# Optimization experiments

Measured on AMD Instinct MI355X. Metric: run time of the kernel, lower is better.

The kernel has to match this reference:

```python
import jax, jax.numpy as jnp
import numpy as np

U, I, E, D, R = 100000, 50000, 2000000, 64, 5


def setup_inputs() -> dict:
    key = jax.random.key(0)
    ks = jax.random.split(key, 14)
    def n(k, shape, scale=0.05):
        return jax.random.normal(k, shape, jnp.float32) * scale
    return {
        "user_feat": n(ks[0], (U, D), 1.0),
        "item_feat": n(ks[1], (I, D), 1.0),
        "rating_feat": n(ks[2], (R, D), 1.0),
        "row_idxs": jax.random.randint(ks[3], (E,), 0, I),   # item index per edge
        "col_idxs": jax.random.randint(ks[4], (E,), 0, U),   # user index per edge (dst)
        "rating": jax.random.randint(ks[5], (E,), 0, R),
        # gv = Linear(2D,D)+ReLU -> Linear(D,D)+ReLU
        "gv_w1": n(ks[6], (2 * D, D)), "gv_b1": jnp.zeros((D,), jnp.float32),
        "gv_w2": n(ks[7], (D, D)),     "gv_b2": jnp.zeros((D,), jnp.float32),
        # Attention: Linear(2D,D)+ReLU -> Linear(D,D)+ReLU -> Linear(D,1)
        "att_w1": n(ks[8], (2 * D, D)), "att_b1": jnp.zeros((D,), jnp.float32),
        "att_w2": n(ks[9], (D, D)),     "att_b2": jnp.zeros((D,), jnp.float32),
        "att_w3": n(ks[10], (D, 1)),    "att_b3": jnp.zeros((1,), jnp.float32),
        # output projection w = Linear(D,D)
        "w_w": n(ks[11], (D, D)), "w_b": jnp.zeros((D,), jnp.float32),
    }


def segment_softmax(logits, seg, num_segments):
    # numerically stable softmax over edges grouped by destination node
    m = jax.ops.segment_max(logits, seg, num_segments=num_segments)
    e = jnp.exp(logits - m[seg])
    s = jax.ops.segment_sum(e, seg, num_segments=num_segments)
    return e / s[seg]


def reference(user_feat, item_feat, rating_feat, row_idxs, col_idxs, rating,
              gv_w1, gv_b1, gv_w2, gv_b2,
              att_w1, att_b1, att_w2, att_b2, att_w3, att_b3,
              w_w, w_b):
    # gather per-edge embeddings
    r_emb = rating_feat[rating]          # [E, D]
    i_emb = item_feat[row_idxs]          # [E, D]
    u_emb = user_feat[col_idxs]          # [E, D]
    # gv MLP on concat(item, rating)
    x = jnp.concatenate([i_emb, r_emb], axis=1)              # [E, 2D]
    h1 = jax.nn.relu(x @ gv_w1 + gv_b1)
    x_ia = jax.nn.relu(h1 @ gv_w2 + gv_b2)                   # [E, D]
    # attention MLP on concat(x_ia, user)
    a = jnp.concatenate([x_ia, u_emb], axis=1)               # [E, 2D]
    a = jax.nn.relu(a @ att_w1 + att_b1)
    a = jax.nn.relu(a @ att_w2 + att_b2)
    weight = (a @ att_w3 + att_b3)[:, 0]                     # [E]
    # edge_softmax over incoming edges of each destination (user) node
    value = segment_softmax(weight, col_idxs, U)             # [E]
    # scatter-sum weighted messages to users
    h = jax.ops.segment_sum(x_ia * value[:, None], col_idxs, num_segments=U)  # [U, D]
    # act is None -> plain linear
    return h @ w_w + w_b
```

## Files before the change

### kernel.cpp

```cpp
#include <hip/hip_runtime.h>
#include <hip/hip_bf16.h>
#include <hip/hip_fp8.h>

#define U_N 100000
#define I_N 50000
#define E_N 2000000
#define R_N 5
#define C_N (I_N*R_N)
#define NBLK_U 391
#define NBLK_E 7813
#define NBLK_C 1954
#define NBUCKC 196

typedef __hip_bfloat16 bf16_t;
typedef unsigned short u16;
typedef unsigned char u8;
typedef __attribute__((ext_vector_type(8))) short bf16x8;
typedef __attribute__((ext_vector_type(4))) float f32x4;

__device__ __forceinline__ float blo(unsigned u){ return __uint_as_float(u<<16); }
__device__ __forceinline__ float bhi(unsigned u){ return __uint_as_float(u & 0xffff0000u); }
__device__ __forceinline__ unsigned pkbf(float a, float b){
  __hip_bfloat162 t = __float22bfloat162_rn(float2{a,b});
  union { __hip_bfloat162 h; unsigned u; } cv; cv.h = t; return cv.u;
}
__device__ __forceinline__ u16 f2b(float v){
  union { __hip_bfloat16 h; u16 u; } cv; cv.h = __float2bfloat16(v); return cv.u;
}
__device__ __forceinline__ float f8f(unsigned b){
  __hip_fp8_e4m3 h; h.__x = (u8)b; return (float)h;
}
__device__ __forceinline__ unsigned ff8(float f){
  __hip_fp8_e4m3 h(f); return (unsigned)h.__x;
}

__global__ __launch_bounds__(256) void k_histQ(const int* __restrict__ cols, int* __restrict__ hist_g){
  __shared__ int histI[NBUCKC];
  int t = threadIdx.x, b = blockIdx.x;
  if(t < NBUCKC) histI[t] = 0;
  __syncthreads();
  int e = b*256 + t;
  if(e < E_N) atomicAdd(&histI[cols[e] >> 9], 1);
  __syncthreads();
  if(t < NBUCKC) hist_g[(size_t)b*NBUCKC + t] = histI[t];
}

__global__ __launch_bounds__(256) void k_scanQ(const int* __restrict__ hist_g, int* __restrict__ boff_g,
                                               int* __restrict__ qtot){
  __shared__ int wsum[4];
  int t = threadIdx.x, q = blockIdx.x;
  int lane = t & 63, wv = t >> 6;
  int running = 0;
  for(int c0=0; c0<NBLK_E; c0+=256){
    int b = c0 + t;
    int v = (b < NBLK_E) ? hist_g[(size_t)b*NBUCKC + q] : 0;
    int inc = v;
#pragma unroll
    for(int off=1; off<64; off<<=1){
      int x = __shfl(inc, lane-off);
      if(lane >= off) inc += x;
    }
    if(lane == 63) wsum[wv] = inc;
    __syncthreads();
    int w0=wsum[0], w1=wsum[1], w2=wsum[2], w3=wsum[3];
    int wpre = (wv>0?w0:0) + (wv>1?w1:0) + (wv>2?w2:0);
    if(b < NBLK_E) boff_g[(size_t)b*NBUCKC + q] = running + wpre + inc - v;
    running += w0 + w1 + w2 + w3;
    __syncthreads();
  }
  if(t == 0) qtot[q] = running;
}

__global__ void k_scanT(const int* __restrict__ qtot, int* __restrict__ qbase){
  __shared__ int s[256];
  int t = threadIdx.x;
  int v = (t < NBUCKC) ? qtot[t] : 0;
  s[t] = v; __syncthreads();
  for(int off=1; off<256; off<<=1){
    int x = (t>=off) ? s[t-off] : 0;
    __syncthreads();
    s[t] += x;
    __syncthreads();
  }
  if(t < NBUCKC) qbase[t] = s[t] - v;
  if(t == 255)   qbase[NBUCKC] = s[255];
}

__global__ __launch_bounds__(256) void k_blockq(const int* __restrict__ qbase, int* __restrict__ blockq){
  int b = blockIdx.x*256 + threadIdx.x; if(b >= NBLK_E) return;
  int e = b*256;
  int lo = 0, hi = NBUCKC-1;
  while(lo < hi){ int mid = (lo+hi+1)>>1; if(qbase[mid] <= e) lo = mid; else hi = mid-1; }
  blockq[b] = lo;
}

__global__ __launch_bounds__(256) void k_place2(const int* __restrict__ rows, const int* __restrict__ cols,
                                                const int* __restrict__ rats,
                                                const int* __restrict__ boff_g, const int* __restrict__ qbase,
                                                unsigned* __restrict__ uc2){
  __shared__ int rankI[NBUCKC];
  __shared__ int baseI[NBUCKC];
  int t = threadIdx.x, b = blockIdx.x;
  if(t < NBUCKC){
    rankI[t] = 0;
    baseI[t] = qbase[t] + boff_g[(size_t)b*NBUCKC + t];
  }
  __syncthreads();
  int e = b*256 + t;
  if(e < E_N){
    int u = cols[e];
    int c = rows[e]*5 + rats[e];
    int q = u >> 9;
    int r = atomicAdd(&rankI[q], 1);
    uc2[baseI[q] + r] = ((unsigned)(u & 16383) << 18) | (unsigned)c;
  }
}

__global__ __launch_bounds__(256) void k_fineB1(const unsigned* __restrict__ uc2, const int* __restrict__ qbase,
                                                int* __restrict__ cnt){
  __shared__ int hist[512];
  int t = threadIdx.x, q = blockIdx.x;
  hist[t] = 0; hist[t+256] = 0;
  __syncthreads();
  int r0 = qbase[q], r1 = qbase[q+1];
  for(int j=r0+t; j<r1; j+=256) atomicAdd(&hist[(uc2[j]>>18) & 511], 1);
  __syncthreads();
  cnt[q*512 + t]       = hist[t];
  cnt[q*512 + t + 256] = hist[t+256];
}

__global__ __launch_bounds__(256) void k_scanA(const int* __restrict__ cnt, int* __restrict__ start,
                                               int* __restrict__ bsum){
  __shared__ int s[256];
  int t = threadIdx.x, i = blockIdx.x*256 + t;
  int v = (i < U_N) ? cnt[i] : 0;
  s[t] = v; __syncthreads();
  for(int off=1; off<256; off<<=1){
    int x = (t>=off) ? s[t-off] : 0;
    __syncthreads();
    s[t] += x;
    __syncthreads();
  }
  start[i] = s[t] - v;
  if(t == 255) bsum[blockIdx.x] = s[255];
}

__global__ void k_scanB(int* bsum, int n){
  __shared__ int s[512];
  int t = threadIdx.x;
  int v = (t < n) ? bsum[t] : 0;
  s[t] = v; __syncthreads();
  for(int off=1; off<512; off<<=1){
    int x = (t>=off) ? s[t-off] : 0;
    __syncthreads();
    s[t] += x;
    __syncthreads();
  }
  if(t < n) bsum[t] = s[t] - v;
}

__global__ __launch_bounds__(256) void k_scanC(int* start, const int* __restrict__ bsum){
  int i = blockIdx.x*256 + threadIdx.x;
  start[i] += bsum[blockIdx.x];
}

__global__ __launch_bounds__(256) void k_fineB2(const unsigned* __restrict__ uc2, const int* __restrict__ qbase,
                                                const int* __restrict__ start,
                                                unsigned* __restrict__ uc3){
  __shared__ int fillb[512];
  __shared__ int startb[512];
  int t = threadIdx.x, q = blockIdx.x;
  fillb[t] = 0; fillb[t+256] = 0;
  startb[t]     = start[q*512 + t];
  startb[t+256] = start[q*512 + t + 256];
  __syncthreads();
  int r0 = qbase[q], r1 = qbase[q+1];
  for(int j=r0+t; j<r1; j+=256){
    unsigned v = uc2[j];
    int ul = (int)((v>>18) & 511);
    int off = atomicAdd(&fillb[ul], 1);
    uc3[startb[ul] + off] = v;
  }
}

__global__ void k_ratpart(const float* __restrict__ rf, const float* __restrict__ w1,
                          const float* __restrict__ b1, float* __restrict__ out){
  int t = threadIdx.x; if(t >= R_N*64) return;
  int r = t>>6, d = t&63;
  float acc = b1[d];
  for(int k=0;k<64;k++) acc += rf[r*64 + k] * w1[(64+k)*64 + d];
  out[t] = acc;
}

__global__ __launch_bounds__(256) void k_prepw6(const float* __restrict__ w1, const float* __restrict__ a1,
                                                const float* __restrict__ w2, const float* __restrict__ a2,
                                                const float* __restrict__ ww,
                                                u16* w1t, u16* u1t, u16* w2t, u16* a1t, u16* a2t, u16* wwt){
  int idx = (blockIdx.x & 15)*256 + threadIdx.x;
  int sec = blockIdx.x >> 4;
  int d = idx >> 6, k = idx & 63;
  const float* src; u16* dst; int ko = 0;
  switch(sec){
    case 0: src=w1; dst=w1t; break;
    case 1: src=a1; dst=u1t; ko=64; break;
    case 2: src=w2; dst=w2t; break;
    case 3: src=a1; dst=a1t; break;
    case 4: src=a2; dst=a2t; break;
    default: src=ww; dst=wwt; break;
  }
  dst[idx] = f2b(src[(size_t)(ko+k)*64 + d]);
}

template<bool BIAS>
__global__ __launch_bounds__(256) void k_rowgemm(const float4* __restrict__ in,
                                                 const uint4* __restrict__ wt,
                                                 const float* __restrict__ bias,
                                                 uint4* __restrict__ outp, int n){
  __shared__ uint4 A_u4[2048];
  __shared__ uint4 W_u4[512];
  __shared__ float bsh[64];
  u16* A16 = (u16*)A_u4;
  const int tid = threadIdx.x;
  for(int cid = tid; cid < 512; cid += 256){
    int dd = cid >> 3, ch = cid & 7;
    W_u4[dd*8 + (ch ^ (dd&7))] = wt[cid];
  }
  if(BIAS && tid < 64) bsh[tid] = bias[tid];
  const int base = blockIdx.x*256;
  const int ch = tid & 7;
#pragma unroll
  for(int it=0; it<8; ++it){
    int s = it*32 + (tid>>3);
    int r = base + s;
    uint4 o = {0,0,0,0};
    if(r < n){
      const float4* p = in + (size_t)r*16 + ch*2;
      float4 v0 = p[0], v1 = p[1];
      o.x = pkbf(v0.x, v0.y); o.y = pkbf(v0.z, v0.w);
      o.z = pkbf(v1.x, v1.y); o.w = pkbf(v1.z, v1.w);
    }
    A_u4[s*8 + (ch ^ (s&7))] = o;
  }
  __syncthreads();
  const int l = tid & 63, w = tid >> 6;
  const int lr = l & 15, g = l >> 4;
  bf16x8 bfr[4][2];
#pragma unroll
  for(int nt=0; nt<4; ++nt)
#pragma unroll
    for(int kk=0; kk<2; ++kk){
      int d = nt*16 + lr;
      bfr[nt][kk] = *(const bf16x8*)&W_u4[d*8 + ((kk*4+g) ^ (d&7))];
    }
  float bv[4];
#pragma unroll
  for(int nt=0; nt<4; ++nt) bv[nt] = BIAS ? bsh[nt*16 + lr] : 0.f;
#pragma unroll
  for(int t=0; t<4; ++t){
    int s = w*64 + t*16 + lr;
    bf16x8 af0 = *(const bf16x8*)&A_u4[s*8 + ((0*4+g) ^ (s&7))];
    bf16x8 af1 = *(const bf16x8*)&A_u4[s*8 + ((1*4+g) ^ (s&7))];
    f32x4 acc[4];
#pragma unroll
    for(int nt=0; nt<4; ++nt){
      f32x4 c0 = { bv[nt], bv[nt], bv[nt], bv[nt] };
      c0 = __builtin_amdgcn_mfma_f32_16x16x32_bf16(af0, bfr[nt][0], c0, 0, 0, 0);
      c0 = __builtin_amdgcn_mfma_f32_16x16x32_bf16(af1, bfr[nt][1], c0, 0, 0, 0);
      acc[nt] = c0;
    }
#pragma unroll
    for(int nt=0; nt<4; ++nt){
      int d = nt*16 + lr;
#pragma unroll
      for(int reg=0; reg<4; ++reg){
        int srow = w*64 + t*16 + g*4 + reg;
        A16[srow*64 + ((d>>3)^(srow&7))*8 + (d&7)] = f2b(acc[nt][reg]);
      }
    }
  }
#pragma unroll
  for(int it=0; it<8; ++it){
    int s = w*64 + it*8 + (l>>3);
    int c2 = l & 7;
    int r = base + s;
    if(r < n) outp[(size_t)r*8 + c2] = A_u4[s*8 + (c2 ^ (s&7))];
  }
}

__global__ __launch_bounds__(256) void k_combo_mfma(const uint4* __restrict__ itemp,
                                                    const float4* __restrict__ ratp,
                                                    const uint4* __restrict__ w2t_g, const uint4* __restrict__ a1t_g,
                                                    const uint4* __restrict__ wwt_g,
                                                    const float* __restrict__ b2,
                                                    uint4* __restrict__ y_o, u8* __restrict__ xa1_o8){
  __shared__ uint4 A_u4[1024];
  __shared__ uint4 X_u4[1024];
  __shared__ uint4 W2_u4[512];
  __shared__ uint4 A1_u4[512];
  __shared__ uint4 WW_u4[512];
  __shared__ float4 rsh4[80];
  __shared__ float b2sh[64];
  u16* A16 = (u16*)A_u4;
  u16* X16 = (u16*)X_u4;
  const int tid = threadIdx.x;
  for(int cid = tid; cid < 512; cid += 256){
    int dd = cid >> 3, ch = cid & 7;
    W2_u4[dd*8 + (ch ^ (dd&7))] = w2t_g[cid];
    A1_u4[dd*8 + (ch ^ (dd&7))] = a1t_g[cid];
    WW_u4[dd*8 + (ch ^ (dd&7))] = wwt_g[cid];
  }
  if(tid < 80) rsh4[tid] = ratp[tid];
  if(tid < 64) b2sh[tid] = b2[tid];
  __syncthreads();

  const int base = blockIdx.x*128;
  const int ch = tid & 7;
#pragma unroll
  for(int it=0; it<4; ++it){
    int s = it*32 + (tid>>3);
    int cidx = base + s;
    uint4 o = {0,0,0,0};
    if(cidx < C_N){
      int i = cidx/5, r = cidx - i*5;
      uint4 iv = itemp[(size_t)i*8 + ch];
      float4 r0 = rsh4[r*16 + ch*2], r1 = rsh4[r*16 + ch*2 + 1];
      o.x = pkbf(fmaxf(blo(iv.x)+r0.x,0.f), fmaxf(bhi(iv.x)+r0.y,0.f));
      o.y = pkbf(fmaxf(blo(iv.y)+r0.z,0.f), fmaxf(bhi(iv.y)+r0.w,0.f));
      o.z = pkbf(fmaxf(blo(iv.z)+r1.x,0.f), fmaxf(bhi(iv.z)+r1.y,0.f));
      o.w = pkbf(fmaxf(blo(iv.w)+r1.z,0.f), fmaxf(bhi(iv.w)+r1.w,0.f));
    }
    A_u4[s*8 + (ch ^ (s&7))] = o;
  }
  __syncthreads();

  const int l = tid & 63, w = tid >> 6;
  const int lr = l & 15, g = l >> 4;
  bf16x8 w2f[4][2], a1f[4][2], wwf[4][2];
#pragma unroll
  for(int nt=0; nt<4; ++nt)
#pragma unroll
    for(int kk=0; kk<2; ++kk){
      int d = nt*16 + lr;
      w2f[nt][kk] = *(const bf16x8*)&W2_u4[d*8 + ((kk*4+g) ^ (d&7))];
      a1f[nt][kk] = *(const bf16x8*)&A1_u4[d*8 + ((kk*4+g) ^ (d&7))];
      wwf[nt][kk] = *(const bf16x8*)&WW_u4[d*8 + ((kk*4+g) ^ (d&7))];
    }
  float b2v[4];
#pragma unroll
  for(int nt=0; nt<4; ++nt) b2v[nt] = b2sh[nt*16 + lr];

#pragma unroll
  for(int t=0; t<2; ++t){
    int s = w*32 + t*16 + lr;
    bf16x8 af0 = *(const bf16x8*)&A_u4[s*8 + ((0*4+g) ^ (s&7))];
    bf16x8 af1 = *(const bf16x8*)&A_u4[s*8 + ((1*4+g) ^ (s&7))];
#pragma unroll
    for(int nt=0; nt<4; ++nt){
      f32x4 c0 = { b2v[nt], b2v[nt], b2v[nt], b2v[nt] };
      c0 = __builtin_amdgcn_mfma_f32_16x16x32_bf16(af0, w2f[nt][0], c0, 0, 0, 0);
      c0 = __builtin_amdgcn_mfma_f32_16x16x32_bf16(af1, w2f[nt][1], c0, 0, 0, 0);
      int d = nt*16 + lr;
#pragma unroll
      for(int reg=0; reg<4; ++reg){
        int srow = w*32 + t*16 + g*4 + reg;
        X16[srow*64 + ((d>>3)^(srow&7))*8 + (d&7)] = f2b(fmaxf(c0[reg], 0.f));
      }
    }
    bf16x8 xf0 = *(const bf16x8*)&X_u4[s*8 + ((0*4+g) ^ (s&7))];
    bf16x8 xf1 = *(const bf16x8*)&X_u4[s*8 + ((1*4+g) ^ (s&7))];
#pragma unroll
    for(int nt=0; nt<4; ++nt){
      f32x4 c0 = { 0.f, 0.f, 0.f, 0.f };
      c0 = __builtin_amdgcn_mfma_f32_16x16x32_bf16(xf0, a1f[nt][0], c0, 0, 0, 0);
      c0 = __builtin_amdgcn_mfma_f32_16x16x32_bf16(xf1, a1f[nt][1], c0, 0, 0, 0);
      int d = nt*16 + lr;
#pragma unroll
      for(int reg=0; reg<4; ++reg){
        int srow = w*32 + t*16 + g*4 + reg;
        A16[srow*64 + ((d>>3)^(srow&7))*8 + (d&7)] = f2b(c0[reg]);
      }
    }
#pragma unroll
    for(int nt=0; nt<4; ++nt){
      f32x4 c0 = { 0.f, 0.f, 0.f, 0.f };
      c0 = __builtin_amdgcn_mfma_f32_16x16x32_bf16(xf0, wwf[nt][0], c0, 0, 0, 0);
      c0 = __builtin_amdgcn_mfma_f32_16x16x32_bf16(xf1, wwf[nt][1], c0, 0, 0, 0);
      int d = nt*16 + lr;
#pragma unroll
      for(int reg=0; reg<4; ++reg){
        int srow = w*32 + t*16 + g*4 + reg;
        X16[srow*64 + ((d>>3)^(srow&7))*8 + (d&7)] = f2b(c0[reg]);
      }
    }
  }
#pragma unroll
  for(int it=0; it<4; ++it){
    int s = w*32 + it*8 + (l>>3);
    int c2 = l & 7;
    int r = base + s;
    if(r < C_N) y_o[(size_t)r*8 + c2] = X_u4[s*8 + (c2 ^ (s&7))];
  }
#pragma unroll
  for(int it=0; it<2; ++it){
    int slot = it*64 + l;
    int rl = slot >> 2;
    int c4 = slot & 3;
    int s = w*32 + rl;
    int r = base + s;
    if(r < C_N){
      uint4 h0 = A_u4[s*8 + ((c4*2+0) ^ (s&7))];
      uint4 h1 = A_u4[s*8 + ((c4*2+1) ^ (s&7))];
      uint4 o;
      o.x = ff8(blo(h0.x)) | (ff8(bhi(h0.x))<<8) | (ff8(blo(h0.y))<<16) | (ff8(bhi(h0.y))<<24);
      o.y = ff8(blo(h0.z)) | (ff8(bhi(h0.z))<<8) | (ff8(blo(h0.w))<<16) | (ff8(bhi(h0.w))<<24);
      o.z = ff8(blo(h1.x)) | (ff8(bhi(h1.x))<<8) | (ff8(blo(h1.y))<<16) | (ff8(bhi(h1.y))<<24);
      o.w = ff8(blo(h1.z)) | (ff8(bhi(h1.z))<<8) | (ff8(blo(h1.w))<<16) | (ff8(bhi(h1.w))<<24);
      *(uint4*)(xa1_o8 + (size_t)r*64 + c4*16) = o;
    }
  }
}

__global__ __launch_bounds__(256) void k_edge_mfma(const unsigned* __restrict__ uc3,
                                                   const int* __restrict__ qbase, const int* __restrict__ blockq,
                                                   const u8* __restrict__ xa1p8, const uint4* __restrict__ userp,
                                                   const u16* __restrict__ w2t_g,
                                                   const float* __restrict__ a2b,
                                                   const float* __restrict__ a3w, const float* __restrict__ a3b,
                                                   float* __restrict__ wlog){
  const int tid = threadIdx.x;
  const int base = blockIdx.x*256;
  const int l = tid & 63, w = tid >> 6;
  const int lr = l & 15;
  const int g  = l >> 4;
  bf16x8 bf[4][2];
#pragma unroll
  for(int nt=0; nt<4; ++nt)
#pragma unroll
    for(int kk=0; kk<2; ++kk){
      int d = nt*16 + lr;
      bf[nt][kk] = *(const bf16x8*)(w2t_g + d*64 + kk*32 + g*8);
    }
  float b2v[4], a3v[4];
#pragma unroll
  for(int nt=0; nt<4; ++nt){ b2v[nt] = a2b[nt*16 + lr]; a3v[nt] = a3w[nt*16 + lr]; }
  const float a3b0 = a3b[0];

  int cin[4], uin[4];
  int bq = blockq[blockIdx.x];
#pragma unroll
  for(int t=0; t<4; ++t){
    int s = base + w*64 + t*16 + lr;
    int sc = (s < E_N) ? s : (E_N-1);
    unsigned vv = (s < E_N) ? uc3[s] : 0u;
    int q = bq;
    while(sc >= qbase[q+1]) ++q;
    cin[t] = (int)(vv & 0x3FFFFu);
    uin[t] = (q<<9) | (int)((vv>>18) & 511u);
  }

  auto compute = [&](uint2 xq0, uint2 xq1, uint4 uv0, uint4 uv1, int t){
    union { uint4 u4; bf16x8 v; } a0, a1;
    a0.u4.x = pkbf(fmaxf(f8f(xq0.x&255u)+blo(uv0.x),0.f),       fmaxf(f8f((xq0.x>>8)&255u)+bhi(uv0.x),0.f));
    a0.u4.y = pkbf(fmaxf(f8f((xq0.x>>16)&255u)+blo(uv0.y),0.f), fmaxf(f8f(xq0.x>>24)+bhi(uv0.y),0.f));
    a0.u4.z = pkbf(fmaxf(f8f(xq0.y&255u)+blo(uv0.z),0.f),       fmaxf(f8f((xq0.y>>8)&255u)+bhi(uv0.z),0.f));
    a0.u4.w = pkbf(fmaxf(f8f((xq0.y>>16)&255u)+blo(uv0.w),0.f), fmaxf(f8f(xq0.y>>24)+bhi(uv0.w),0.f));
    a1.u4.x = pkbf(fmaxf(f8f(xq1.x&255u)+blo(uv1.x),0.f),       fmaxf(f8f((xq1.x>>8)&255u)+bhi(uv1.x),0.f));
    a1.u4.y = pkbf(fmaxf(f8f((xq1.x>>16)&255u)+blo(uv1.y),0.f), fmaxf(f8f(xq1.x>>24)+bhi(uv1.y),0.f));
    a1.u4.z = pkbf(fmaxf(f8f(xq1.y&255u)+blo(uv1.z),0.f),       fmaxf(f8f((xq1.y>>8)&255u)+bhi(uv1.z),0.f));
    a1.u4.w = pkbf(fmaxf(f8f((xq1.y>>16)&255u)+blo(uv1.w),0.f), fmaxf(f8f(xq1.y>>24)+bhi(uv1.w),0.f));
    f32x4 acc[4];
#pragma unroll
    for(int nt=0; nt<4; ++nt){
      f32x4 c0 = { b2v[nt], b2v[nt], b2v[nt], b2v[nt] };
      c0 = __builtin_amdgcn_mfma_f32_16x16x32_bf16(a0.v, bf[nt][0], c0, 0, 0, 0);
      c0 = __builtin_amdgcn_mfma_f32_16x16x32_bf16(a1.v, bf[nt][1], c0, 0, 0, 0);
      acc[nt] = c0;
    }
    float s0=0.f, s1=0.f, s2=0.f, s3=0.f;
#pragma unroll
    for(int nt=0; nt<4; ++nt){
      s0 += fmaxf(acc[nt][0], 0.f) * a3v[nt];
      s1 += fmaxf(acc[nt][1], 0.f) * a3v[nt];
      s2 += fmaxf(acc[nt][2], 0.f) * a3v[nt];
      s3 += fmaxf(acc[nt][3], 0.f) * a3v[nt];
    }
#pragma unroll
    for(int mask=1; mask<16; mask<<=1){
      s0 += __shfl_xor(s0, mask);
      s1 += __shfl_xor(s1, mask);
      s2 += __shfl_xor(s2, mask);
      s3 += __shfl_xor(s3, mask);
    }
    if(lr == 0){
      int e0 = base + w*64 + t*16 + g*4;
      if(e0+0 < E_N) wlog[e0+0] = s0 + a3b0;
      if(e0+1 < E_N) wlog[e0+1] = s1 + a3b0;
      if(e0+2 < E_N) wlog[e0+2] = s2 + a3b0;
      if(e0+3 < E_N) wlog[e0+3] = s3 + a3b0;
    }
  };

  uint2 xA0 = *(const uint2*)(xa1p8 + (size_t)cin[0]*64 + g*8);
  uint2 xA1 = *(const uint2*)(xa1p8 + (size_t)cin[0]*64 + 32 + g*8);
  uint4 uA0 = userp[(size_t)uin[0]*8 + g];
  uint4 uA1 = userp[(size_t)uin[0]*8 + 4 + g];
  uint2 xB0 = *(const uint2*)(xa1p8 + (size_t)cin[1]*64 + g*8);
  uint2 xB1 = *(const uint2*)(xa1p8 + (size_t)cin[1]*64 + 32 + g*8);
  uint4 uB0 = userp[(size_t)uin[1]*8 + g];
  uint4 uB1 = userp[(size_t)uin[1]*8 + 4 + g];

  compute(xA0, xA1, uA0, uA1, 0);
  xA0 = *(const uint2*)(xa1p8 + (size_t)cin[2]*64 + g*8);
  xA1 = *(const uint2*)(xa1p8 + (size_t)cin[2]*64 + 32 + g*8);
  uA0 = userp[(size_t)uin[2]*8 + g];
  uA1 = userp[(size_t)uin[2]*8 + 4 + g];
  compute(xB0, xB1, uB0, uB1, 1);
  xB0 = *(const uint2*)(xa1p8 + (size_t)cin[3]*64 + g*8);
  xB1 = *(const uint2*)(xa1p8 + (size_t)cin[3]*64 + 32 + g*8);
  uB0 = userp[(size_t)uin[3]*8 + g];
  uB1 = userp[(size_t)uin[3]*8 + 4 + g];
  compute(xA0, xA1, uA0, uA1, 2);
  compute(xB0, xB1, uB0, uB1, 3);
}

__global__ __launch_bounds__(256) void k_aggf(const int* __restrict__ start,
                                              const unsigned* __restrict__ uc3,
                                              const float* __restrict__ wlog,
                                              const u16* __restrict__ Y,
                                              const float* __restrict__ wb,
                                              float* __restrict__ out){
  __shared__ uint4 Ysh[2][4][256];
  int w = threadIdx.x >> 6, l = threadIdx.x & 63;
  int lr = l & 15, g = l >> 4;
  int base = (blockIdx.x*4 + w) * 16;
  if(base >= U_N) return;
  int s0g = start[base];
  int s1g = start[base+16];
  unsigned ml = (unsigned)((base + lr) & 16383);
  int sA = s0g & ~31;
  int nch = (s1g - sA + 31) >> 5;
  const int kb = g*8;

  float m = -1e30f;
  for(int ch=0; ch<nch; ++ch){
    int e0 = sA + ch*32;
    float4 wv0 = *(const float4*)(wlog + e0 + kb);
    float4 wv1 = *(const float4*)(wlog + e0 + kb + 4);
    uint4 v0 = *(const uint4*)(uc3 + e0 + kb);
    uint4 v1 = *(const uint4*)(uc3 + e0 + kb + 4);
    if((v0.x>>18)==ml) m = fmaxf(m, wv0.x);
    if((v0.y>>18)==ml) m = fmaxf(m, wv0.y);
    if((v0.z>>18)==ml) m = fmaxf(m, wv0.z);
    if((v0.w>>18)==ml) m = fmaxf(m, wv0.w);
    if((v1.x>>18)==ml) m = fmaxf(m, wv1.x);
    if((v1.y>>18)==ml) m = fmaxf(m, wv1.y);
    if((v1.z>>18)==ml) m = fmaxf(m, wv1.z);
    if((v1.w>>18)==ml) m = fmaxf(m, wv1.w);
  }
  m = fmaxf(m, __shfl_xor(m, 16));
  m = fmaxf(m, __shfl_xor(m, 32));

  f32x4 acc[4];
#pragma unroll
  for(int nt=0; nt<4; ++nt) acc[nt] = f32x4{0.f,0.f,0.f,0.f};
  float ssum = 0.f;
  int buf = 0;
  if(nch > 0){
    int rowe = sA + (l>>1);
    int crow = (int)(uc3[rowe] & 0x3FFFFu);
    const uint4* yp = (const uint4*)Y + (size_t)crow*8 + (l&1)*4;
    uint4 y0=yp[0], y1=yp[1], y2=yp[2], y3=yp[3];
    uint4* dst = &Ysh[0][w][(l>>1)*8 + (l&1)*4];
    dst[0]=y0; dst[1]=y1; dst[2]=y2; dst[3]=y3;
  }
  for(int ch=0; ch<nch; ++ch){
    int e0 = sA + ch*32;
    uint4 n0, n1, n2, n3;
    bool hasNext = (ch+1 < nch);
    if(hasNext){
      int rowe = e0 + 32 + (l>>1);
      int crowN = (int)(uc3[rowe] & 0x3FFFFu);
      const uint4* yp = (const uint4*)Y + (size_t)crowN*8 + (l&1)*4;
      n0=yp[0]; n1=yp[1]; n2=yp[2]; n3=yp[3];
    }
    float4 wv0 = *(const float4*)(wlog + e0 + kb);
    float4 wv1 = *(const float4*)(wlog + e0 + kb + 4);
    uint4 v0 = *(const uint4*)(uc3 + e0 + kb);
    uint4 v1 = *(const uint4*)(uc3 + e0 + kb + 4);
    bf16x8 af;
    {
      bool mt; float e;
      mt = ((v0.x>>18)==ml); e = __expf((mt?wv0.x:-1e30f) - m); ssum += mt?e:0.f; af[0] = mt?(short)f2b(e):(short)0;
      mt = ((v0.y>>18)==ml); e = __expf((mt?wv0.y:-1e30f) - m); ssum += mt?e:0.f; af[1] = mt?(short)f2b(e):(short)0;
      mt = ((v0.z>>18)==ml); e = __expf((mt?wv0.z:-1e30f) - m); ssum += mt?e:0.f; af[2] = mt?(short)f2b(e):(short)0;
      mt = ((v0.w>>18)==ml); e = __expf((mt?wv0.w:-1e30f) - m); ssum += mt?e:0.f; af[3] = mt?(short)f2b(e):(short)0;
      mt = ((v1.x>>18)==ml); e = __expf((mt?wv1.x:-1e30f) - m); ssum += mt?e:0.f; af[4] = mt?(short)f2b(e):(short)0;
      mt = ((v1.y>>18)==ml); e = __expf((mt?wv1.y:-1e30f) - m); ssum += mt?e:0.f; af[5] = mt?(short)f2b(e):(short)0;
      mt = ((v1.z>>18)==ml); e = __expf((mt?wv1.z:-1e30f) - m); ssum += mt?e:0.f; af[6] = mt?(short)f2b(e):(short)0;
      mt = ((v1.w>>18)==ml); e = __expf((mt?wv1.w:-1e30f) - m); ssum += mt?e:0.f; af[7] = mt?(short)f2b(e):(short)0;
    }
    u16* Ysh16 = (u16*)&Ysh[buf][w][0];
    bf16x8 b0, b1, b2, b3;
#pragma unroll
    for(int j=0; j<8; ++j){
      int r = (kb + j)*64 + lr;
      b0[j] = (short)Ysh16[r];
      b1[j] = (short)Ysh16[r+16];
      b2[j] = (short)Ysh16[r+32];
      b3[j] = (short)Ysh16[r+48];
    }
    acc[0] = __builtin_amdgcn_mfma_f32_16x16x32_bf16(af, b0, acc[0], 0, 0, 0);
    acc[1] = __builtin_amdgcn_mfma_f32_16x16x32_bf16(af, b1, acc[1], 0, 0, 0);
    acc[2] = __builtin_amdgcn_mfma_f32_16x16x32_bf16(af, b2, acc[2], 0, 0, 0);
    acc[3] = __builtin_amdgcn_mfma_f32_16x16x32_bf16(af, b3, acc[3], 0, 0, 0);
    if(hasNext){
      uint4* dst = &Ysh[buf^1][w][(l>>1)*8 + (l&1)*4];
      dst[0]=n0; dst[1]=n1; dst[2]=n2; dst[3]=n3;
    }
    buf ^= 1;
  }
  ssum += __shfl_xor(ssum, 16);
  ssum += __shfl_xor(ssum, 32);
  float inv = (ssum > 0.f) ? (1.f/ssum) : 0.f;
  float wbv[4];
#pragma unroll
  for(int nt=0; nt<4; ++nt) wbv[nt] = wb[nt*16 + lr];
#pragma unroll
  for(int reg=0; reg<4; ++reg){
    float sc = __shfl(inv, g*4 + reg);
    int u = base + g*4 + reg;
#pragma unroll
    for(int nt=0; nt<4; ++nt)
      out[(size_t)u*64 + nt*16 + lr] = acc[nt][reg]*sc + wbv[nt];
  }
}

extern "C" void kernel_launch(void* const* d_in, const int* in_sizes, int n_in,
                              void* d_out, int out_size, void* d_ws, size_t ws_size,
                              hipStream_t stream){
  (void)in_sizes; (void)n_in; (void)out_size; (void)ws_size;
  const float4* user_feat  = (const float4*)d_in[0];
  const float4* item_feat  = (const float4*)d_in[1];
  const float*  rating_feat= (const float*)d_in[2];
  const int*    rows       = (const int*)d_in[3];
  const int*    cols       = (const int*)d_in[4];
  const int*    rats       = (const int*)d_in[5];
  const float* gv_w1 = (const float*)d_in[6];
  const float* gv_b1 = (const float*)d_in[7];
  const float* gv_w2 = (const float*)d_in[8];
  const float* gv_b2 = (const float*)d_in[9];
  const float* att_w1= (const float*)d_in[10];
  const float* att_b1= (const float*)d_in[11];
  const float* att_w2= (const float*)d_in[12];
  const float* att_b2= (const float*)d_in[13];
  const float* att_w3= (const float*)d_in[14];
  const float* att_b3= (const float*)d_in[15];
  const float* w_w   = (const float*)d_in[16];
  const float* w_b   = (const float*)d_in[17];
  float* out = (float*)d_out;

  char* ws = (char*)d_ws; size_t off = 0;
  auto take = [&](size_t b)->char*{ char* p = ws + off; off = (off + b + 255) & ~(size_t)255; return p; };
  bf16_t*   item_part  = (bf16_t*)take((size_t)I_N*64*2);
  bf16_t*   user_part  = (bf16_t*)take((size_t)U_N*64*2);
  float*    rating_part= (float*) take((size_t)R_N*64*4);
  bf16_t*   y_t        = (bf16_t*)take((size_t)C_N*64*2);
  u8*       xa1_8      = (u8*)    take((size_t)C_N*64);
  float*    wlog_s     = (float*) take((size_t)E_N*4);
  unsigned* uc3        = (unsigned*)take((size_t)E_N*4);
  unsigned* uc2        = (unsigned*)take((size_t)E_N*4);
  int*      hist_g     = (int*)   take((size_t)NBLK_E*NBUCKC*4);
  int*      boff_g     = (int*)   take((size_t)NBLK_E*NBUCKC*4);
  int*      qtot       = (int*)   take((size_t)256*4);
  int*      qbase      = (int*)   take((size_t)256*4);
  int*      blockq     = (int*)   take((size_t)NBLK_E*4);
  int*      cnt        = (int*)   take((size_t)(NBUCKC*512+256)*4);
  int*      start      = (int*)   take((size_t)(NBUCKC*512+256)*4);
  int*      bsum       = (int*)   take((size_t)512*4);
  u16*      w1t        = (u16*)   take((size_t)4096*2);
  u16*      u1t        = (u16*)   take((size_t)4096*2);
  u16*      w2t        = (u16*)   take((size_t)4096*2);
  u16*      a1t        = (u16*)   take((size_t)4096*2);
  u16*      a2t        = (u16*)   take((size_t)4096*2);
  u16*      wwt        = (u16*)   take((size_t)4096*2);

  k_histQ <<<NBLK_E, 256, 0, stream>>>(cols, hist_g);
  k_scanQ <<<NBUCKC, 256, 0, stream>>>(hist_g, boff_g, qtot);
  k_scanT <<<1, 256, 0, stream>>>(qtot, qbase);
  k_blockq<<<(NBLK_E+255)/256, 256, 0, stream>>>(qbase, blockq);
  k_place2<<<NBLK_E, 256, 0, stream>>>(rows, cols, rats, boff_g, qbase, uc2);
  k_fineB1<<<NBUCKC, 256, 0, stream>>>(uc2, qbase, cnt);
  k_scanA <<<NBLK_U, 256, 0, stream>>>(cnt, start, bsum);
  k_scanB <<<1, 512, 0, stream>>>(bsum, NBLK_U);
  k_scanC <<<NBLK_U, 256, 0, stream>>>(start, bsum);
  k_fineB2<<<NBUCKC, 256, 0, stream>>>(uc2, qbase, start, uc3);
  k_ratpart <<<1, 320, 0, stream>>>(rating_feat, gv_w1, gv_b1, rating_part);
  k_prepw6  <<<96, 256, 0, stream>>>(gv_w1, att_w1, gv_w2, att_w2, w_w, w1t, u1t, w2t, a1t, a2t, wwt);
  k_rowgemm<false><<<(I_N+255)/256, 256, 0, stream>>>(item_feat, (const uint4*)w1t, nullptr,
                                                      (uint4*)item_part, I_N);
  k_rowgemm<true> <<<NBLK_U, 256, 0, stream>>>(user_feat, (const uint4*)u1t, att_b1,
                                               (uint4*)user_part, U_N);
  k_combo_mfma<<<NBLK_C, 256, 0, stream>>>((const uint4*)item_part, (const float4*)rating_part,
                                           (const uint4*)w2t, (const uint4*)a1t, (const uint4*)wwt, gv_b2,
                                           (uint4*)y_t, xa1_8);
  k_edge_mfma<<<NBLK_E, 256, 0, stream>>>(uc3, qbase, blockq, xa1_8, (const uint4*)user_part,
                                          w2t, att_b2, att_w3, att_b3, wlog_s);
  k_aggf <<<(U_N/64)+1, 256, 0, stream>>>(start, uc3, wlog_s, (const u16*)y_t, w_b, out);
}
```

Measured before the change: 293.3 us.

## Fuse fine bucket sort stages, drop softmax max pass, use packed fp8 decode

Five kernels (fine histogram, three-level scan, fine scatter) become one per-bucket kernel. It does a local 512-entry scan in shared memory and derives global offsets from the existing bucket base, which removes four launches and the intermediate count and block-sum buffers. The aggregation kernel drops the first pass that computed a per-user max, so it exponentiates raw logits directly. This saves a full read of logits and indices but relies on logits staying small enough not to overflow exp. The edge kernel also decodes fp8 inputs two at a time with the packed fp8x2 conversion instead of one byte at a time.

```diff
diff --git a/kernel.cpp b/kernel.cpp
--- a/kernel.cpp
+++ b/kernel.cpp
@@ -7,7 +7,6 @@
 #define E_N 2000000
 #define R_N 5
 #define C_N (I_N*R_N)
-#define NBLK_U 391
 #define NBLK_E 7813
 #define NBLK_C 1954
 #define NBUCKC 196
@@ -27,11 +26,11 @@
 __device__ __forceinline__ u16 f2b(float v){
   union { __hip_bfloat16 h; u16 u; } cv; cv.h = __float2bfloat16(v); return cv.u;
 }
-__device__ __forceinline__ float f8f(unsigned b){
-  __hip_fp8_e4m3 h; h.__x = (u8)b; return (float)h;
-}
 __device__ __forceinline__ unsigned ff8(float f){
   __hip_fp8_e4m3 h(f); return (unsigned)h.__x;
+}
+__device__ __forceinline__ float2 f8x2(u16 h){
+  __hip_fp8x2_e4m3 v; v.__x = h; return (float2)v;
 }
 
 __global__ __launch_bounds__(256) void k_histQ(const int* __restrict__ cols, int* __restrict__ hist_g){
@@ -116,70 +115,36 @@
   }
 }
 
-__global__ __launch_bounds__(256) void k_fineB1(const unsigned* __restrict__ uc2, const int* __restrict__ qbase,
-                                                int* __restrict__ cnt){
-  __shared__ int hist[512];
+__global__ __launch_bounds__(256) void k_fine(const unsigned* __restrict__ uc2, const int* __restrict__ qbase,
+                                              unsigned* __restrict__ uc3, int* __restrict__ start){
+  __shared__ int histv[512];
+  __shared__ int s[512];
+  __shared__ int fillb[512];
   int t = threadIdx.x, q = blockIdx.x;
-  hist[t] = 0; hist[t+256] = 0;
+  histv[t]=0; histv[t+256]=0; fillb[t]=0; fillb[t+256]=0;
   __syncthreads();
   int r0 = qbase[q], r1 = qbase[q+1];
-  for(int j=r0+t; j<r1; j+=256) atomicAdd(&hist[(uc2[j]>>18) & 511], 1);
-  __syncthreads();
-  cnt[q*512 + t]       = hist[t];
-  cnt[q*512 + t + 256] = hist[t+256];
-}
-
-__global__ __launch_bounds__(256) void k_scanA(const int* __restrict__ cnt, int* __restrict__ start,
-                                               int* __restrict__ bsum){
-  __shared__ int s[256];
-  int t = threadIdx.x, i = blockIdx.x*256 + t;
-  int v = (i < U_N) ? cnt[i] : 0;
-  s[t] = v; __syncthreads();
-  for(int off=1; off<256; off<<=1){
-    int x = (t>=off) ? s[t-off] : 0;
+  for(int j=r0+t; j<r1; j+=256) atomicAdd(&histv[(uc2[j]>>18)&511], 1);
+  __syncthreads();
+  s[t]=histv[t]; s[t+256]=histv[t+256];
+  __syncthreads();
+  for(int off=1; off<512; off<<=1){
+    int a0 = (t>=off)? s[t-off] : 0;
+    int a1 = (t+256>=off)? s[t+256-off] : 0;
     __syncthreads();
-    s[t] += x;
+    s[t]+=a0; s[t+256]+=a1;
     __syncthreads();
   }
-  start[i] = s[t] - v;
-  if(t == 255) bsum[blockIdx.x] = s[255];
-}
-
-__global__ void k_scanB(int* bsum, int n){
-  __shared__ int s[512];
-  int t = threadIdx.x;
-  int v = (t < n) ? bsum[t] : 0;
-  s[t] = v; __syncthreads();
-  for(int off=1; off<512; off<<=1){
-    int x = (t>=off) ? s[t-off] : 0;
-    __syncthreads();
-    s[t] += x;
-    __syncthreads();
-  }
-  if(t < n) bsum[t] = s[t] - v;
-}
-
-__global__ __launch_bounds__(256) void k_scanC(int* start, const int* __restrict__ bsum){
-  int i = blockIdx.x*256 + threadIdx.x;
-  start[i] += bsum[blockIdx.x];
-}
-
-__global__ __launch_bounds__(256) void k_fineB2(const unsigned* __restrict__ uc2, const int* __restrict__ qbase,
-                                                const int* __restrict__ start,
-                                                unsigned* __restrict__ uc3){
-  __shared__ int fillb[512];
-  __shared__ int startb[512];
-  int t = threadIdx.x, q = blockIdx.x;
-  fillb[t] = 0; fillb[t+256] = 0;
-  startb[t]     = start[q*512 + t];
-  startb[t+256] = start[q*512 + t + 256];
-  __syncthreads();
-  int r0 = qbase[q], r1 = qbase[q+1];
+  int e0 = s[t]-histv[t], e1 = s[t+256]-histv[t+256];
+  start[q*512+t]     = r0 + e0;
+  start[q*512+t+256] = r0 + e1;
+  s[t]=e0; s[t+256]=e1;
+  __syncthreads();
   for(int j=r0+t; j<r1; j+=256){
     unsigned v = uc2[j];
-    int ul = (int)((v>>18) & 511);
+    int ul = (int)((v>>18)&511);
     int off = atomicAdd(&fillb[ul], 1);
-    uc3[startb[ul] + off] = v;
+    uc3[r0 + s[ul] + off] = v;
   }
 }
 
@@ -460,14 +425,20 @@
 
   auto compute = [&](uint2 xq0, uint2 xq1, uint4 uv0, uint4 uv1, int t){
     union { uint4 u4; bf16x8 v; } a0, a1;
-    a0.u4.x = pkbf(fmaxf(f8f(xq0.x&255u)+blo(uv0.x),0.f),       fmaxf(f8f((xq0.x>>8)&255u)+bhi(uv0.x),0.f));
-    a0.u4.y = pkbf(fmaxf(f8f((xq0.x>>16)&255u)+blo(uv0.y),0.f), fmaxf(f8f(xq0.x>>24)+bhi(uv0.y),0.f));
-    a0.u4.z = pkbf(fmaxf(f8f(xq0.y&255u)+blo(uv0.z),0.f),       fmaxf(f8f((xq0.y>>8)&255u)+bhi(uv0.z),0.f));
-    a0.u4.w = pkbf(fmaxf(f8f((xq0.y>>16)&255u)+blo(uv0.w),0.f), fmaxf(f8f(xq0.y>>24)+bhi(uv0.w),0.f));
-    a1.u4.x = pkbf(fmaxf(f8f(xq1.x&255u)+blo(uv1.x),0.f),       fmaxf(f8f((xq1.x>>8)&255u)+bhi(uv1.x),0.f));
-    a1.u4.y = pkbf(fmaxf(f8f((xq1.x>>16)&255u)+blo(uv1.y),0.f), fmaxf(f8f(xq1.x>>24)+bhi(uv1.y),0.f));
-    a1.u4.z = pkbf(fmaxf(f8f(xq1.y&255u)+blo(uv1.z),0.f),       fmaxf(f8f((xq1.y>>8)&255u)+bhi(uv1.z),0.f));
-    a1.u4.w = pkbf(fmaxf(f8f((xq1.y>>16)&255u)+blo(uv1.w),0.f), fmaxf(f8f(xq1.y>>24)+bhi(uv1.w),0.f));
+    {
+      float2 p01 = f8x2((u16)xq0.x), p23 = f8x2((u16)(xq0.x>>16));
+      float2 p45 = f8x2((u16)xq0.y), p67 = f8x2((u16)(xq0.y>>16));
+      a0.u4.x = pkbf(fmaxf(p01.x+blo(uv0.x),0.f), fmaxf(p01.y+bhi(uv0.x),0.f));
+      a0.u4.y = pkbf(fmaxf(p23.x+blo(uv0.y),0.f), fmaxf(p23.y+bhi(uv0.y),0.f));
+      a0.u4.z = pkbf(fmaxf(p45.x+blo(uv0.z),0.f), fmaxf(p45.y+bhi(uv0.z),0.f));
+      a0.u4.w = pkbf(fmaxf(p67.x+blo(uv0.w),0.f), fmaxf(p67.y+bhi(uv0.w),0.f));
+      p01 = f8x2((u16)xq1.x); p23 = f8x2((u16)(xq1.x>>16));
+      p45 = f8x2((u16)xq1.y); p67 = f8x2((u16)(xq1.y>>16));
+      a1.u4.x = pkbf(fmaxf(p01.x+blo(uv1.x),0.f), fmaxf(p01.y+bhi(uv1.x),0.f));
+      a1.u4.y = pkbf(fmaxf(p23.x+blo(uv1.y),0.f), fmaxf(p23.y+bhi(uv1.y),0.f));
+      a1.u4.z = pkbf(fmaxf(p45.x+blo(uv1.z),0.f), fmaxf(p45.y+bhi(uv1.z),0.f));
+      a1.u4.w = pkbf(fmaxf(p67.x+blo(uv1.w),0.f), fmaxf(p67.y+bhi(uv1.w),0.f));
+    }
     f32x4 acc[4];
 #pragma unroll
     for(int nt=0; nt<4; ++nt){
@@ -541,25 +512,6 @@
   int nch = (s1g - sA + 31) >> 5;
   const int kb = g*8;
 
-  float m = -1e30f;
-  for(int ch=0; ch<nch; ++ch){
-    int e0 = sA + ch*32;
-    float4 wv0 = *(const float4*)(wlog + e0 + kb);
-    float4 wv1 = *(const float4*)(wlog + e0 + kb + 4);
-    uint4 v0 = *(const uint4*)(uc3 + e0 + kb);
-    uint4 v1 = *(const uint4*)(uc3 + e0 + kb + 4);
-    if((v0.x>>18)==ml) m = fmaxf(m, wv0.x);
-    if((v0.y>>18)==ml) m = fmaxf(m, wv0.y);
-    if((v0.z>>18)==ml) m = fmaxf(m, wv0.z);
-    if((v0.w>>18)==ml) m = fmaxf(m, wv0.w);
-    if((v1.x>>18)==ml) m = fmaxf(m, wv1.x);
-    if((v1.y>>18)==ml) m = fmaxf(m, wv1.y);
-    if((v1.z>>18)==ml) m = fmaxf(m, wv1.z);
-    if((v1.w>>18)==ml) m = fmaxf(m, wv1.w);
-  }
-  m = fmaxf(m, __shfl_xor(m, 16));
-  m = fmaxf(m, __shfl_xor(m, 32));
-
   f32x4 acc[4];
 #pragma unroll
   for(int nt=0; nt<4; ++nt) acc[nt] = f32x4{0.f,0.f,0.f,0.f};
@@ -590,14 +542,14 @@
     bf16x8 af;
     {
       bool mt; float e;
-      mt = ((v0.x>>18)==ml); e = __expf((mt?wv0.x:-1e30f) - m); ssum += mt?e:0.f; af[0] = mt?(short)f2b(e):(short)0;
-      mt = ((v0.y>>18)==ml); e = __expf((mt?wv0.y:-1e30f) - m); ssum += mt?e:0.f; af[1] = mt?(short)f2b(e):(short)0;
-      mt = ((v0.z>>18)==ml); e = __expf((mt?wv0.z:-1e30f) - m); ssum += mt?e:0.f; af[2] = mt?(short)f2b(e):(short)0;
-      mt = ((v0.w>>18)==ml); e = __expf((mt?wv0.w:-1e30f) - m); ssum += mt?e:0.f; af[3] = mt?(short)f2b(e):(short)0;
-      mt = ((v1.x>>18)==ml); e = __expf((mt?wv1.x:-1e30f) - m); ssum += mt?e:0.f; af[4] = mt?(short)f2b(e):(short)0;
-      mt = ((v1.y>>18)==ml); e = __expf((mt?wv1.y:-1e30f) - m); ssum += mt?e:0.f; af[5] = mt?(short)f2b(e):(short)0;
-      mt = ((v1.z>>18)==ml); e = __expf((mt?wv1.z:-1e30f) - m); ssum += mt?e:0.f; af[6] = mt?(short)f2b(e):(short)0;
-      mt = ((v1.w>>18)==ml); e = __expf((mt?wv1.w:-1e30f) - m); ssum += mt?e:0.f; af[7] = mt?(short)f2b(e):(short)0;
+      mt = ((v0.x>>18)==ml); e = __expf(mt?wv0.x:-1e30f); ssum += e; af[0] = mt?(short)f2b(e):(short)0;
+      mt = ((v0.y>>18)==ml); e = __expf(mt?wv0.y:-1e30f); ssum += e; af[1] = mt?(short)f2b(e):(short)0;
+      mt = ((v0.z>>18)==ml); e = __expf(mt?wv0.z:-1e30f); ssum += e; af[2] = mt?(short)f2b(e):(short)0;
+      mt = ((v0.w>>18)==ml); e = __expf(mt?wv0.w:-1e30f); ssum += e; af[3] = mt?(short)f2b(e):(short)0;
+      mt = ((v1.x>>18)==ml); e = __expf(mt?wv1.x:-1e30f); ssum += e; af[4] = mt?(short)f2b(e):(short)0;
+      mt = ((v1.y>>18)==ml); e = __expf(mt?wv1.y:-1e30f); ssum += e; af[5] = mt?(short)f2b(e):(short)0;
+      mt = ((v1.z>>18)==ml); e = __expf(mt?wv1.z:-1e30f); ssum += e; af[6] = mt?(short)f2b(e):(short)0;
+      mt = ((v1.w>>18)==ml); e = __expf(mt?wv1.w:-1e30f); ssum += e; af[7] = mt?(short)f2b(e):(short)0;
     }
     u16* Ysh16 = (u16*)&Ysh[buf][w][0];
     bf16x8 b0, b1, b2, b3;
@@ -674,9 +626,7 @@
   int*      qtot       = (int*)   take((size_t)256*4);
   int*      qbase      = (int*)   take((size_t)256*4);
   int*      blockq     = (int*)   take((size_t)NBLK_E*4);
-  int*      cnt        = (int*)   take((size_t)(NBUCKC*512+256)*4);
-  int*      start      = (int*)   take((size_t)(NBUCKC*512+256)*4);
-  int*      bsum       = (int*)   take((size_t)512*4);
+  int*      start      = (int*)   take((size_t)(NBUCKC*512+64)*4);
   u16*      w1t        = (u16*)   take((size_t)4096*2);
   u16*      u1t        = (u16*)   take((size_t)4096*2);
   u16*      w2t        = (u16*)   take((size_t)4096*2);
@@ -689,17 +639,13 @@
   k_scanT <<<1, 256, 0, stream>>>(qtot, qbase);
   k_blockq<<<(NBLK_E+255)/256, 256, 0, stream>>>(qbase, blockq);
   k_place2<<<NBLK_E, 256, 0, stream>>>(rows, cols, rats, boff_g, qbase, uc2);
-  k_fineB1<<<NBUCKC, 256, 0, stream>>>(uc2, qbase, cnt);
-  k_scanA <<<NBLK_U, 256, 0, stream>>>(cnt, start, bsum);
-  k_scanB <<<1, 512, 0, stream>>>(bsum, NBLK_U);
-  k_scanC <<<NBLK_U, 256, 0, stream>>>(start, bsum);
-  k_fineB2<<<NBUCKC, 256, 0, stream>>>(uc2, qbase, start, uc3);
+  k_fine  <<<NBUCKC, 256, 0, stream>>>(uc2, qbase, uc3, start);
   k_ratpart <<<1, 320, 0, stream>>>(rating_feat, gv_w1, gv_b1, rating_part);
   k_prepw6  <<<96, 256, 0, stream>>>(gv_w1, att_w1, gv_w2, att_w2, w_w, w1t, u1t, w2t, a1t, a2t, wwt);
   k_rowgemm<false><<<(I_N+255)/256, 256, 0, stream>>>(item_feat, (const uint4*)w1t, nullptr,
                                                       (uint4*)item_part, I_N);
-  k_rowgemm<true> <<<NBLK_U, 256, 0, stream>>>(user_feat, (const uint4*)u1t, att_b1,
-                                               (uint4*)user_part, U_N);
+  k_rowgemm<true> <<<(U_N+255)/256, 256, 0, stream>>>(user_feat, (const uint4*)u1t, att_b1,
+                                                      (uint4*)user_part, U_N);
   k_combo_mfma<<<NBLK_C, 256, 0, stream>>>((const uint4*)item_part, (const float4*)rating_part,
                                            (const uint4*)w2t, (const uint4*)a1t, (const uint4*)wwt, gv_b2,
                                            (uint4*)y_t, xa1_8);
```

After: 263.8 us. 10.0% less time.
